# Kernel optimization log

Hardware: AMD Instinct MI355X
Metric: run time of the kernel (lower is better)

## Reference

```python
import math
import jax, jax.numpy as jnp
import numpy as np

WINDOW = 2  # LocalAttention default window_size
EPS = 1e-6


def _linear(x, W, b):
    return x @ W + b


def local_attention(x, Wq, bq, Wk, bk, Wv, bv):
    # x: [B, S, D]
    B, S, D = x.shape
    q = _linear(x, Wq, bq)
    k = _linear(x, Wk, bk)
    v = _linear(x, Wv, bv)
    idx = jnp.arange(S)
    # 0/1 banded mask -> softmax gives a dense row-stochastic matrix (faithful to source)
    mask = (jnp.abs(idx[:, None] - idx[None, :]) <= WINDOW).astype(x.dtype)  # [S, S]
    A = jax.nn.softmax(mask, axis=-1)  # [S, S]
    kk = jnp.einsum('st,btd->bsd', A, k)  # bmm(A, k)
    scores = jnp.einsum('bsd,btd->bst', q, kk) / math.sqrt(D)
    return jnp.einsum('bst,btd->bsd', jax.nn.softmax(scores, axis=-1), v)


def whole_norm(x, w, b):
    # LayerNorm with normalized_shape == full [B, S, D]: normalize over ALL elements
    mu = jnp.mean(x)
    var = jnp.mean(jnp.square(x - mu))
    return (x - mu) * jax.lax.rsqrt(var + EPS) * w + b


def ffn(x, W1, b1, W2, b2):
    return _linear(jax.nn.relu(_linear(x, W1, b1)), W2, b2)


def branch(feat, Wq, bq, Wk, bk, Wv, bv, W1, b1, W2, b2, nw, nb):
    out = local_attention(feat, Wq, bq, Wk, bk, Wv, bv)
    out = whole_norm(out + feat, nw, nb)
    out = ffn(out, W1, b1, W2, b2)
    return whole_norm(out + feat, nw, nb)


def _make_params(key, B, S, D):
    ks = jax.random.split(key, 5)
    s = 1.0 / math.sqrt(D)
    Wq = jax.random.normal(ks[0], (D, D), jnp.float32) * s
    Wk = jax.random.normal(ks[1], (D, D), jnp.float32) * s
    Wv = jax.random.normal(ks[2], (D, D), jnp.float32) * s
    W1 = jax.random.normal(ks[3], (D, 4 * D), jnp.float32) * s
    W2 = jax.random.normal(ks[4], (4 * D, D), jnp.float32) * (1.0 / math.sqrt(4 * D))
    return dict(Wq=Wq, bq=jnp.zeros((D,)), Wk=Wk, bk=jnp.zeros((D,)),
                Wv=Wv, bv=jnp.zeros((D,)), W1=W1, b1=jnp.zeros((4 * D,)),
                W2=W2, b2=jnp.zeros((D,)), nw=jnp.ones((B, S, D)), nb=jnp.zeros((B, S, D)))


def setup_inputs() -> dict:
    key = jax.random.key(0)
    k0, k1, k2, k3 = jax.random.split(key, 4)
    B, St, Dt = 8, 512, 1024
    Si, Di = 196, 768
    inp = {
        'text_feature': jax.random.normal(k0, (B, St, Dt), jnp.float32),
        'image_feature': jax.random.normal(k1, (B, Si, Di), jnp.float32),
    }
    tp = _make_params(k2, B, St, Dt)
    ip = _make_params(k3, B, Si, Di)
    for k, v in tp.items():
        inp['t_' + k] = v
    for k, v in ip.items():
        inp['i_' + k] = v
    return inp


def reference(text_feature, image_feature,
              t_Wq, t_bq, t_Wk, t_bk, t_Wv, t_bv, t_W1, t_b1, t_W2, t_b2, t_nw, t_nb,
              i_Wq, i_bq, i_Wk, i_bk, i_Wv, i_bv, i_W1, i_b1, i_W2, i_b2, i_nw, i_nb):
    image_out = branch(image_feature, i_Wq, i_bq, i_Wk, i_bk, i_Wv, i_bv,
                       i_W1, i_b1, i_W2, i_b2, i_nw, i_nb)
    text_out = branch(text_feature, t_Wq, t_bq, t_Wk, t_bk, t_Wv, t_bv,
                      t_W1, t_b1, t_W2, t_b2, t_nw, t_nb)
    return (text_out, image_out)
```

## Files before the change

### kernel.cpp

```cpp
#include <hip/hip_runtime.h>
#include <math.h>

typedef float  f32x4  __attribute__((ext_vector_type(4)));
typedef short  bf16x8 __attribute__((ext_vector_type(8)));

__device__ __forceinline__ unsigned short f2bf(float f) {
    union { float f; unsigned u; } v; v.f = f;
    unsigned u = v.u;
    return (unsigned short)((u + 0x7FFFu + ((u >> 16) & 1u)) >> 16);
}
__device__ __forceinline__ float bf2f(unsigned short u) {
    union { unsigned u; float f; } v; v.u = (unsigned)u << 16; return v.f;
}

#define GLOAD_LDS16(g, l)                                                      \
    __builtin_amdgcn_global_load_lds(                                          \
        (const __attribute__((address_space(1))) void*)(g),                    \
        (__attribute__((address_space(3))) void*)(l), 16, 0, 0)

template<int WRW, int WCW, int MR, int NR, bool OUT_BF16, bool RELU>
__global__ __launch_bounds__(512, 2)
void gemm5_bf16(const unsigned short* __restrict__ A,
                const unsigned short* __restrict__ BT,
                const float* __restrict__ bias, void* __restrict__ Cv,
                int M, int N, int K, int lda, int ldb, int ldc,
                long long sA, long long sB, long long sC, float alpha,
                int gx, int gy)
{
    constexpr int BK = 64;
    constexpr int WM = MR * 16, WN = NR * 16;
    constexpr int BM = WRW * WM, BN = WCW * WN;
    constexpr int NL = (BM + BN) / 64;
    __shared__ unsigned short Asm[2][BM * BK];
    __shared__ unsigned short Bsm[2][BN * BK];

    A  += (long long)blockIdx.z * sA;
    BT += (long long)blockIdx.z * sB;
    char* Cb = (char*)Cv + (long long)blockIdx.z * sC * (OUT_BF16 ? 2 : 4);

    const int nwg = gx * gy;
    int orig = blockIdx.x;
    int xcd = orig & 7, sidx = orig >> 3;
    int qq = nwg >> 3, rr = nwg & 7;
    int wg = (xcd < rr ? xcd * (qq + 1) : rr * (qq + 1) + (xcd - rr) * qq) + sidx;
    const int row0 = (wg / gx) * BM;
    const int col0 = (wg % gx) * BN;

    const int tid  = threadIdx.x;
    const int lane = tid & 63;
    const int wave = tid >> 6;
    const int wr   = wave / WCW;
    const int wc   = wave % WCW;

    const int lrow = lane & 15;
    const int cgrp = lane >> 4;

    f32x4 acc[MR][NR] = {};

    const int srl = tid >> 3;
    const int scl = (tid & 7) ^ (srl & 7);

    auto stage = [&](int buf, int k0) {
        #pragma unroll
        for (int is = 0; is < BM / 64; ++is)
            GLOAD_LDS16(A + (long long)(row0 + is * 64 + srl) * lda + (k0 + scl * 8),
                        &Asm[buf][is * 64 * BK + tid * 8]);
        #pragma unroll
        for (int is = 0; is < BN / 64; ++is)
            GLOAD_LDS16(BT + (long long)(col0 + is * 64 + srl) * ldb + (k0 + scl * 8),
                        &Bsm[buf][is * 64 * BK + tid * 8]);
    };

    const int nt = K / BK;
    stage(0, 0);

    for (int t = 0; t < nt; ++t) {
        const int cur = t & 1;
        if (t + 1 < nt) {
            stage(cur ^ 1, (t + 1) * BK);
            if constexpr (NL == 8)      asm volatile("s_waitcnt vmcnt(8)" ::: "memory");
            else if constexpr (NL == 6) asm volatile("s_waitcnt vmcnt(6)" ::: "memory");
            else                        asm volatile("s_waitcnt vmcnt(0)" ::: "memory");
        } else {
            asm volatile("s_waitcnt vmcnt(0)" ::: "memory");
        }
        __builtin_amdgcn_s_barrier();
        __builtin_amdgcn_sched_barrier(0);

        #pragma unroll
        for (int kk = 0; kk < 2; ++kk) {
            bf16x8 a_[MR], b_[NR];
            #pragma unroll
            for (int mf = 0; mf < MR; ++mf) {
                int row = wr * WM + mf * 16 + lrow;
                int phys = (kk * 4 + cgrp) ^ (row & 7);
                a_[mf] = *(const bf16x8*)&Asm[cur][row * BK + phys * 8];
            }
            #pragma unroll
            for (int nf = 0; nf < NR; ++nf) {
                int row = wc * WN + nf * 16 + lrow;
                int phys = (kk * 4 + cgrp) ^ (row & 7);
                b_[nf] = *(const bf16x8*)&Bsm[cur][row * BK + phys * 8];
            }
            __builtin_amdgcn_s_setprio(1);
            #pragma unroll
            for (int mf = 0; mf < MR; ++mf)
                #pragma unroll
                for (int nf = 0; nf < NR; ++nf)
                    acc[mf][nf] = __builtin_amdgcn_mfma_f32_16x16x32_bf16(
                        a_[mf], b_[nf], acc[mf][nf], 0, 0, 0);
            __builtin_amdgcn_s_setprio(0);
        }
        __builtin_amdgcn_s_barrier();
    }

    const int crow = cgrp * 4;
    const int ccol = lane & 15;
    #pragma unroll
    for (int mf = 0; mf < MR; ++mf) {
        int rbase = row0 + wr * WM + mf * 16 + crow;
        #pragma unroll
        for (int nf = 0; nf < NR; ++nf) {
            int c = col0 + wc * WN + nf * 16 + ccol;
            if (c >= N) continue;
            float bv = bias ? bias[c] : 0.f;
            #pragma unroll
            for (int j = 0; j < 4; ++j) {
                int r = rbase + j;
                if (r >= M) continue;
                float v = acc[mf][nf][j] * alpha + bv;
                if (RELU) v = fmaxf(v, 0.f);
                if (OUT_BF16)
                    ((unsigned short*)Cb)[(long long)r * ldc + c] = f2bf(v);
                else
                    ((float*)Cb)[(long long)r * ldc + c] = v;
            }
        }
    }
}

template<int WRW, int WCW, int MR, int NR>
static void gemm5_t(bool outBf16, bool relu,
                    const unsigned short* A, const unsigned short* BT, const float* bias,
                    void* C, int M, int N, int K, int lda, int ldb, int ldc,
                    int batch, long long sA, long long sB, long long sC,
                    float alpha, hipStream_t st)
{
    const int BM = WRW * MR * 16, BN = WCW * NR * 16;
    int gx = (N + BN - 1) / BN, gy = (M + BM - 1) / BM;
    dim3 grid(gx * gy, 1, batch);
    if (outBf16) {
        if (relu) gemm5_bf16<WRW, WCW, MR, NR, true , true ><<<grid, 512, 0, st>>>(A, BT, bias, C, M, N, K, lda, ldb, ldc, sA, sB, sC, alpha, gx, gy);
        else      gemm5_bf16<WRW, WCW, MR, NR, true , false><<<grid, 512, 0, st>>>(A, BT, bias, C, M, N, K, lda, ldb, ldc, sA, sB, sC, alpha, gx, gy);
    } else {
        if (relu) gemm5_bf16<WRW, WCW, MR, NR, false, true ><<<grid, 512, 0, st>>>(A, BT, bias, C, M, N, K, lda, ldb, ldc, sA, sB, sC, alpha, gx, gy);
        else      gemm5_bf16<WRW, WCW, MR, NR, false, false><<<grid, 512, 0, st>>>(A, BT, bias, C, M, N, K, lda, ldb, ldc, sA, sB, sC, alpha, gx, gy);
    }
}

template<int MR, int NR, bool OUT_BF16, bool RELU>
__global__ __launch_bounds__(512, 4)
void gemm4_bf16(const unsigned short* __restrict__ A,
                const unsigned short* __restrict__ BT,
                const float* __restrict__ bias, void* __restrict__ Cv,
                int M, int N, int K, int lda, int ldb, int ldc,
                long long sA, long long sB, long long sC, float alpha,
                int gx, int gy)
{
    constexpr int BK = 64;
    constexpr int WM = MR * 16, WN = NR * 16;
    constexpr int BM = 2 * WM, BN = 4 * WN;
    __shared__ unsigned short Asm[2][BM * BK];
    __shared__ unsigned short Bsm[2][BN * BK];

    A  += (long long)blockIdx.z * sA;
    BT += (long long)blockIdx.z * sB;
    char* Cb = (char*)Cv + (long long)blockIdx.z * sC * (OUT_BF16 ? 2 : 4);

    const int nwg = gx * gy;
    int orig = blockIdx.x;
    int xcd = orig & 7, sidx = orig >> 3;
    int qq = nwg >> 3, rr = nwg & 7;
    int wg = (xcd < rr ? xcd * (qq + 1) : rr * (qq + 1) + (xcd - rr) * qq) + sidx;
    const int row0 = (wg / gx) * BM;
    const int col0 = (wg % gx) * BN;

    const int tid  = threadIdx.x;
    const int lane = tid & 63;
    const int wave = tid >> 6;
    const int wr   = wave >> 2;
    const int wc   = wave & 3;

    const int lrow = lane & 15;
    const int cgrp = lane >> 4;

    f32x4 acc[MR][NR] = {};

    const int srl = tid >> 3;
    const int scl = (tid & 7) ^ (srl & 7);

    auto stage = [&](int buf, int k0) {
        #pragma unroll
        for (int is = 0; is < BM / 64; ++is)
            GLOAD_LDS16(A + (long long)(row0 + is * 64 + srl) * lda + (k0 + scl * 8),
                        &Asm[buf][is * 64 * BK + tid * 8]);
        #pragma unroll
        for (int is = 0; is < BN / 64; ++is)
            GLOAD_LDS16(BT + (long long)(col0 + is * 64 + srl) * ldb + (k0 + scl * 8),
                        &Bsm[buf][is * 64 * BK + tid * 8]);
    };

    const int nt = K / BK;
    stage(0, 0);
    __syncthreads();

    for (int t = 0; t < nt; ++t) {
        if (t + 1 < nt) stage((t + 1) & 1, (t + 1) * BK);
        const int cur = t & 1;

        bf16x8 a_[2][MR], b_[2][NR];
        #pragma unroll
        for (int kk = 0; kk < 2; ++kk) {
            #pragma unroll
            for (int mf = 0; mf < MR; ++mf) {
                int row = wr * WM + mf * 16 + lrow;
                int phys = (kk * 4 + cgrp) ^ (row & 7);
                a_[kk][mf] = *(const bf16x8*)&Asm[cur][row * BK + phys * 8];
            }
            #pragma unroll
            for (int nf = 0; nf < NR; ++nf) {
                int row = wc * WN + nf * 16 + lrow;
                int phys = (kk * 4 + cgrp) ^ (row & 7);
                b_[kk][nf] = *(const bf16x8*)&Bsm[cur][row * BK + phys * 8];
            }
        }

        __builtin_amdgcn_s_setprio(1);
        #pragma unroll
        for (int kk = 0; kk < 2; ++kk)
            #pragma unroll
            for (int mf = 0; mf < MR; ++mf)
                #pragma unroll
                for (int nf = 0; nf < NR; ++nf)
                    acc[mf][nf] = __builtin_amdgcn_mfma_f32_16x16x32_bf16(
                        a_[kk][mf], b_[kk][nf], acc[mf][nf], 0, 0, 0);
        __builtin_amdgcn_s_setprio(0);

        __syncthreads();
    }

    const int crow = cgrp * 4;
    const int ccol = lane & 15;
    #pragma unroll
    for (int mf = 0; mf < MR; ++mf) {
        int rbase = row0 + wr * WM + mf * 16 + crow;
        #pragma unroll
        for (int nf = 0; nf < NR; ++nf) {
            int c = col0 + wc * WN + nf * 16 + ccol;
            if (c >= N) continue;
            float bv = bias ? bias[c] : 0.f;
            #pragma unroll
            for (int j = 0; j < 4; ++j) {
                int r = rbase + j;
                if (r >= M) continue;
                float v = acc[mf][nf][j] * alpha + bv;
                if (RELU) v = fmaxf(v, 0.f);
                if (OUT_BF16)
                    ((unsigned short*)Cb)[(long long)r * ldc + c] = f2bf(v);
                else
                    ((float*)Cb)[(long long)r * ldc + c] = v;
            }
        }
    }
}

template<int MR, int NR>
static void gemm4_t(bool outBf16, bool relu,
                    const unsigned short* A, const unsigned short* BT, const float* bias,
                    void* C, int M, int N, int K, int lda, int ldb, int ldc,
                    int batch, long long sA, long long sB, long long sC,
                    float alpha, hipStream_t st)
{
    const int BM = 2 * MR * 16, BN = 4 * NR * 16;
    int gx = (N + BN - 1) / BN, gy = (M + BM - 1) / BM;
    dim3 grid(gx * gy, 1, batch);
    if (outBf16) {
        if (relu) gemm4_bf16<MR, NR, true , true ><<<grid, 512, 0, st>>>(A, BT, bias, C, M, N, K, lda, ldb, ldc, sA, sB, sC, alpha, gx, gy);
        else      gemm4_bf16<MR, NR, true , false><<<grid, 512, 0, st>>>(A, BT, bias, C, M, N, K, lda, ldb, ldc, sA, sB, sC, alpha, gx, gy);
    } else {
        if (relu) gemm4_bf16<MR, NR, false, true ><<<grid, 512, 0, st>>>(A, BT, bias, C, M, N, K, lda, ldb, ldc, sA, sB, sC, alpha, gx, gy);
        else      gemm4_bf16<MR, NR, false, false><<<grid, 512, 0, st>>>(A, BT, bias, C, M, N, K, lda, ldb, ldc, sA, sB, sC, alpha, gx, gy);
    }
}

template<int BM, int BN, bool OUT_BF16>
__global__ __launch_bounds__(256)
void gemm_bf16(const unsigned short* __restrict__ A,
               const unsigned short* __restrict__ BT,
               const float* __restrict__ bias, void* __restrict__ Cv,
               int M, int N, int K, int lda, int ldb, int ldc,
               long long sA, long long sB, long long sC, float alpha,
               int gx, int gy)
{
    constexpr int BK = 32;
    constexpr int WM = BM / 2, WN = BN / 2;
    constexpr int MR = WM / 16, NR = WN / 16;
    __shared__ unsigned short Asm[BM * BK];
    __shared__ unsigned short Bsm[BN * BK];

    A  += (long long)blockIdx.z * sA;
    BT += (long long)blockIdx.z * sB;
    char* Cb = (char*)Cv + (long long)blockIdx.z * sC * (OUT_BF16 ? 2 : 4);

    const int nwg = gx * gy;
    int orig = blockIdx.x;
    int xcd = orig & 7, sidx = orig >> 3;
    int qq = nwg >> 3, rr = nwg & 7;
    int wg = (xcd < rr ? xcd * (qq + 1) : rr * (qq + 1) + (xcd - rr) * qq) + sidx;
    const int row0 = (wg % gy) * BM;
    const int col0 = (wg / gy) * BN;

    const int tid  = threadIdx.x;
    const int lane = tid & 63;
    const int wave = tid >> 6;
    const int wr   = wave >> 1;
    const int wc   = wave & 1;

    const int srow = tid >> 2;
    const int skel = (tid & 3) * 8;

    f32x4 acc[MR][NR] = {};

    const int lrow = lane & 15;
    const int lk   = (lane >> 4) * 8;

    for (int k0 = 0; k0 < K; k0 += BK) {
        #pragma unroll
        for (int is = 0; is < BM / 64; ++is)
            GLOAD_LDS16(A + (long long)(row0 + is * 64 + srow) * lda + (k0 + skel),
                        &Asm[(is * 64 + srow) * BK + skel]);
        #pragma unroll
        for (int is = 0; is < BN / 64; ++is)
            GLOAD_LDS16(BT + (long long)(col0 + is * 64 + srow) * ldb + (k0 + skel),
                        &Bsm[(is * 64 + srow) * BK + skel]);
        __syncthreads();

        bf16x8 af[MR], bfr[NR];
        #pragma unroll
        for (int mf = 0; mf < MR; ++mf)
            af[mf] = *(const bf16x8*)&Asm[(wr * WM + mf * 16 + lrow) * BK + lk];
        #pragma unroll
        for (int nf = 0; nf < NR; ++nf)
            bfr[nf] = *(const bf16x8*)&Bsm[(wc * WN + nf * 16 + lrow) * BK + lk];
        #pragma unroll
        for (int mf = 0; mf < MR; ++mf)
            #pragma unroll
            for (int nf = 0; nf < NR; ++nf)
                acc[mf][nf] = __builtin_amdgcn_mfma_f32_16x16x32_bf16(
                    af[mf], bfr[nf], acc[mf][nf], 0, 0, 0);
        __syncthreads();
    }

    const int crow = (lane >> 4) * 4;
    const int ccol = lane & 15;
    #pragma unroll
    for (int mf = 0; mf < MR; ++mf) {
        int rbase = row0 + wr * WM + mf * 16 + crow;
        #pragma unroll
        for (int nf = 0; nf < NR; ++nf) {
            int c = col0 + wc * WN + nf * 16 + ccol;
            if (c >= N) continue;
            float bv = bias ? bias[c] : 0.f;
            #pragma unroll
            for (int j = 0; j < 4; ++j) {
                int r = rbase + j;
                if (r >= M) continue;
                float v = acc[mf][nf][j] * alpha + bv;
                if (OUT_BF16)
                    ((unsigned short*)Cb)[(long long)r * ldc + c] = f2bf(v);
                else
                    ((float*)Cb)[(long long)r * ldc + c] = v;
            }
        }
    }
}

template<int BM, int BN>
static void gemm_t(bool outBf16,
                   const unsigned short* A, const unsigned short* BT, const float* bias,
                   void* C, int M, int N, int K, int lda, int ldb, int ldc,
                   int batch, long long sA, long long sB, long long sC,
                   float alpha, hipStream_t st)
{
    int gx = (N + BN - 1) / BN, gy = (M + BM - 1) / BM;
    dim3 grid(gx * gy, 1, batch);
    if (outBf16)
        gemm_bf16<BM, BN, true ><<<grid, 256, 0, st>>>(A, BT, bias, C, M, N, K, lda, ldb, ldc, sA, sB, sC, alpha, gx, gy);
    else
        gemm_bf16<BM, BN, false><<<grid, 256, 0, st>>>(A, BT, bias, C, M, N, K, lda, ldb, ldc, sA, sB, sC, alpha, gx, gy);
}

__global__ void splitk_stats_kernel(const float4* __restrict__ part,
                                    const float4* __restrict__ bias,
                                    const float4* __restrict__ x,
                                    float4* __restrict__ z,
                                    double* __restrict__ dpart,
                                    long long n4, int N4, int nsplit, long long stride4)
{
    __shared__ double rs[256], rs2[256];
    int tid = threadIdx.x;
    long long i = (long long)blockIdx.x * blockDim.x + tid;
    long long gs = (long long)gridDim.x * blockDim.x;
    double s = 0.0, s2 = 0.0;
    for (; i < n4; i += gs) {
        float4 a = part[i];
        for (int sp = 1; sp < nsplit; ++sp) {
            float4 b = part[(long long)sp * stride4 + i];
            a.x += b.x; a.y += b.y; a.z += b.z; a.w += b.w;
        }
        float4 bv = bias[(int)(i % N4)];
        float4 xv = x[i];
        a.x += bv.x + xv.x; a.y += bv.y + xv.y; a.z += bv.z + xv.z; a.w += bv.w + xv.w;
        z[i] = a;
        s  += (double)a.x + (double)a.y + (double)a.z + (double)a.w;
        s2 += (double)a.x * a.x + (double)a.y * a.y + (double)a.z * a.z + (double)a.w * a.w;
    }
    rs[tid] = s; rs2[tid] = s2; __syncthreads();
    for (int k = 128; k > 0; k >>= 1) {
        if (tid < k) { rs[tid] += rs[tid + k]; rs2[tid] += rs2[tid + k]; }
        __syncthreads();
    }
    if (tid == 0) { dpart[2 * blockIdx.x] = rs[0]; dpart[2 * blockIdx.x + 1] = rs2[0]; }
}

__global__ void norm_apply_z_kernel(const float4* __restrict__ z,
                                    const float4* __restrict__ nw, const float4* __restrict__ nb,
                                    const float* __restrict__ stats, float4* __restrict__ out,
                                    long long n4)
{
    float mu = stats[0], rstd = stats[1];
    long long i = (long long)blockIdx.x * blockDim.x + threadIdx.x;
    long long stride = (long long)gridDim.x * blockDim.x;
    for (; i < n4; i += stride) {
        float4 zv = z[i], wv = nw[i], bv = nb[i];
        float4 o;
        o.x = (zv.x - mu) * rstd * wv.x + bv.x;
        o.y = (zv.y - mu) * rstd * wv.y + bv.y;
        o.z = (zv.z - mu) * rstd * wv.z + bv.z;
        o.w = (zv.w - mu) * rstd * wv.w + bv.w;
        out[i] = o;
    }
}

__global__ void cast_bf16_kernel(const float4* __restrict__ in,
                                 ushort4* __restrict__ out, long long n4)
{
    long long i = (long long)blockIdx.x * blockDim.x + threadIdx.x;
    long long stride = (long long)gridDim.x * blockDim.x;
    for (; i < n4; i += stride) {
        float4 v = in[i];
        ushort4 o;
        o.x = f2bf(v.x); o.y = f2bf(v.y); o.z = f2bf(v.z); o.w = f2bf(v.w);
        out[i] = o;
    }
}

__global__ void transpose_cast_kernel(const float* __restrict__ src,
                                      unsigned short* __restrict__ dst,
                                      int R, int C, int Rpad,
                                      long long sSrc, long long sDst)
{
    __shared__ float t[32][33];
    src += (long long)blockIdx.z * sSrc;
    dst += (long long)blockIdx.z * sDst;
    int r0 = blockIdx.x * 32, c0 = blockIdx.y * 32;
    int tx = threadIdx.x & 31, ty = threadIdx.x >> 5;
    #pragma unroll
    for (int i = 0; i < 32; i += 8) {
        int r = r0 + ty + i, c = c0 + tx;
        t[ty + i][tx] = (r < R && c < C) ? src[(long long)r * C + c] : 0.f;
    }
    __syncthreads();
    #pragma unroll
    for (int i = 0; i < 32; i += 8) {
        int c = c0 + ty + i, r = r0 + tx;
        if (c < C && r < Rpad)
            dst[(long long)c * Rpad + r] = f2bf(t[tx][ty + i]);
    }
}

__global__ void transpose_bf16_kernel(const unsigned short* __restrict__ src,
                                      unsigned short* __restrict__ dst,
                                      int R, int C, int Rpad, int ldS,
                                      long long sSrc, long long sDst)
{
    __shared__ unsigned short t[32][33];
    src += (long long)blockIdx.z * sSrc;
    dst += (long long)blockIdx.z * sDst;
    int r0 = blockIdx.x * 32, c0 = blockIdx.y * 32;
    int tx = threadIdx.x & 31, ty = threadIdx.x >> 5;
    #pragma unroll
    for (int i = 0; i < 32; i += 8) {
        int r = r0 + ty + i, c = c0 + tx;
        t[ty + i][tx] = (r < R && c < C) ? src[(long long)r * ldS + c] : (unsigned short)0;
    }
    __syncthreads();
    #pragma unroll
    for (int i = 0; i < 32; i += 8) {
        int c = c0 + ty + i, r = r0 + tx;
        if (c < C && r < Rpad)
            dst[(long long)c * Rpad + r] = t[tx][ty + i];
    }
}

#define KTOT_NCH 16
__global__ void ktot_partial_bf16(const unsigned short* __restrict__ k,
                                  float* __restrict__ part,
                                  int B, int S, int D, int ld)
{
    int bch = blockIdx.x;
    int b  = bch / KTOT_NCH;
    int ch = bch % KTOT_NCH;
    int d  = blockIdx.y * 256 + threadIdx.x;
    if (d >= D) return;
    int len = (S + KTOT_NCH - 1) / KTOT_NCH;
    int lo = ch * len;
    int hi = lo + len < S ? lo + len : S;
    const unsigned short* kp = k + ((long long)b * S + lo) * ld + d;
    float s = 0.f;
    for (int t = lo; t < hi; ++t, kp += ld) s += bf2f(*kp);
    part[(long long)bch * D + d] = s;
}

__global__ void ktot_finish_kernel(const float* __restrict__ part,
                                   float* __restrict__ ktot, int B, int D)
{
    int idx = blockIdx.x * blockDim.x + threadIdx.x;
    if (idx >= B * D) return;
    int b = idx / D, d = idx % D;
    float s = 0.f;
    #pragma unroll
    for (int ch = 0; ch < KTOT_NCH; ++ch)
        s += part[((long long)b * KTOT_NCH + ch) * D + d];
    ktot[idx] = s;
}

__global__ void kk_bf16_kernel(const unsigned short* __restrict__ k,
                               const float* __restrict__ ktot,
                               unsigned short* __restrict__ kk,
                               int B, int S, int D, int ld)
{
    long long idx = (long long)blockIdx.x * blockDim.x + threadIdx.x;
    int D4 = D >> 2;
    long long n4 = (long long)B * S * D4;
    if (idx >= n4) return;
    int d4 = (int)(idx % D4);
    long long bs = idx / D4;
    int s = (int)(bs % S);
    int b = (int)(bs / S);
    int lo = s - 2 > 0 ? s - 2 : 0;
    int hi = s + 2 < S - 1 ? s + 2 : S - 1;
    int c = hi - lo + 1;
    const float E = 2.718281828459045f;
    float Zinv = 1.f / ((float)(S - c) + E * (float)c);

    float w0 = 0.f, w1 = 0.f, w2 = 0.f, w3 = 0.f;
    const unsigned short* kp = k + ((long long)b * S + lo) * ld + d4 * 4;
    for (int t = lo; t <= hi; ++t, kp += ld) {
        ushort4 kv = *(const ushort4*)kp;
        w0 += bf2f(kv.x); w1 += bf2f(kv.y); w2 += bf2f(kv.z); w3 += bf2f(kv.w);
    }
    float4 tot = *((const float4*)(ktot + b * D) + d4);
    ushort4 o;
    o.x = f2bf((tot.x + (E - 1.f) * w0) * Zinv);
    o.y = f2bf((tot.y + (E - 1.f) * w1) * Zinv);
    o.z = f2bf((tot.z + (E - 1.f) * w2) * Zinv);
    o.w = f2bf((tot.w + (E - 1.f) * w3) * Zinv);
    ((ushort4*)(kk + ((long long)b * S + s) * D))[d4] = o;
}

__global__ void softmax_rows_bf16(const float* __restrict__ sc,
                                  unsigned short* __restrict__ P, int S, int Spad)
{
    long long row = blockIdx.x;
    const float* p = sc + row * (long long)Spad;
    unsigned short* o = P + row * (long long)Spad;
    int tid = threadIdx.x;
    __shared__ float red[256];

    float m = -INFINITY;
    for (int t = tid; t < S; t += 256) m = fmaxf(m, p[t]);
    red[tid] = m; __syncthreads();
    for (int s = 128; s > 0; s >>= 1) {
        if (tid < s) red[tid] = fmaxf(red[tid], red[tid + s]);
        __syncthreads();
    }
    m = red[0];
    __syncthreads();

    float sum = 0.f;
    for (int t = tid; t < S; t += 256) sum += __expf(p[t] - m);
    red[tid] = sum; __syncthreads();
    for (int s = 128; s > 0; s >>= 1) {
        if (tid < s) red[tid] += red[tid + s];
        __syncthreads();
    }
    float inv = 1.f / red[0];
    for (int t = tid; t < Spad; t += 256)
        o[t] = (t < S) ? f2bf(__expf(p[t] - m) * inv) : (unsigned short)0;
}

__global__ void stats_kernel(const float4* __restrict__ a, const float4* __restrict__ f,
                             double* __restrict__ part, long long n4)
{
    __shared__ double rs[256], rs2[256];
    int tid = threadIdx.x;
    long long i = (long long)blockIdx.x * blockDim.x + tid;
    long long stride = (long long)gridDim.x * blockDim.x;
    double s = 0.0, s2 = 0.0;
    for (; i < n4; i += stride) {
        float4 av = a[i], fv = f[i];
        float z0 = av.x + fv.x, z1 = av.y + fv.y, z2 = av.z + fv.z, z3 = av.w + fv.w;
        s  += (double)z0 + (double)z1 + (double)z2 + (double)z3;
        s2 += (double)z0 * z0 + (double)z1 * z1 + (double)z2 * z2 + (double)z3 * z3;
    }
    rs[tid] = s; rs2[tid] = s2; __syncthreads();
    for (int k = 128; k > 0; k >>= 1) {
        if (tid < k) { rs[tid] += rs[tid + k]; rs2[tid] += rs2[tid + k]; }
        __syncthreads();
    }
    if (tid == 0) { part[2 * blockIdx.x] = rs[0]; part[2 * blockIdx.x + 1] = rs2[0]; }
}

__global__ void finish_stats(const double* __restrict__ part, int npart,
                             float* __restrict__ stats, double n)
{
    __shared__ double rs[256], rs2[256];
    int tid = threadIdx.x;
    double s = 0.0, s2 = 0.0;
    for (int i = tid; i < npart; i += 256) { s += part[2 * i]; s2 += part[2 * i + 1]; }
    rs[tid] = s; rs2[tid] = s2; __syncthreads();
    for (int k = 128; k > 0; k >>= 1) {
        if (tid < k) { rs[tid] += rs[tid + k]; rs2[tid] += rs2[tid + k]; }
        __syncthreads();
    }
    if (tid == 0) {
        double mu  = rs[0] / n;
        double var = rs2[0] / n - mu * mu;
        stats[0] = (float)mu;
        stats[1] = (float)(1.0 / sqrt(var + 1e-6));
    }
}

__global__ void norm_apply_kernel(const float4* __restrict__ a, const float4* __restrict__ f,
                                  const float4* __restrict__ nw, const float4* __restrict__ nb,
                                  const float* __restrict__ stats, ushort4* __restrict__ out,
                                  long long n4)
{
    float mu = stats[0], rstd = stats[1];
    long long i = (long long)blockIdx.x * blockDim.x + threadIdx.x;
    long long stride = (long long)gridDim.x * blockDim.x;
    for (; i < n4; i += stride) {
        float4 av = a[i], fv = f[i], wv = nw[i], bv = nb[i];
        ushort4 o;
        o.x = f2bf((av.x + fv.x - mu) * rstd * wv.x + bv.x);
        o.y = f2bf((av.y + fv.y - mu) * rstd * wv.y + bv.y);
        o.z = f2bf((av.z + fv.z - mu) * rstd * wv.z + bv.z);
        o.w = f2bf((av.w + fv.w - mu) * rstd * wv.w + bv.w);
        out[i] = o;
    }
}

struct Bufs {
    unsigned short *xb, *qkv, *kkb, *vT, *P, *h, *WqkvT, *W1T, *W2T;
    float *f32buf, *bqkv, *ktot, *ktot_part, *stats;
    double *part;
};

static void run_branch(const float* x, const float* const* w, bool big,
                       float* out, int B, int S, int D, const Bufs& wsb, hipStream_t st)
{
    const float *Wq = w[0], *bq = w[1], *Wk = w[2], *bk = w[3], *Wv = w[4], *bv = w[5];
    const float *W1 = w[6], *b1 = w[7], *W2 = w[8], *b2 = w[9], *nw = w[10], *nb = w[11];

    const int Spad = (S + 31) & ~31;
    const long long M = (long long)B * S;
    const long long n = M * D;
    const long long n4 = n / 4;
    const float inv_sqrt_d = (float)(1.0 / sqrt((double)D));
    const int D3 = 3 * D, D4 = 4 * D;

    unsigned short* y1b = wsb.kkb;
    float* scores = (float*)wsb.h;
    float* splitbuf = (float*)wsb.qkv;

    cast_bf16_kernel<<<1024, 256, 0, st>>>((const float4*)x, (ushort4*)wsb.xb, n4);
    transpose_cast_kernel<<<dim3((D + 31) / 32, (D + 31) / 32, 1), 256, 0, st>>>(Wq, wsb.WqkvT,               D, D, D, 0, 0);
    transpose_cast_kernel<<<dim3((D + 31) / 32, (D + 31) / 32, 1), 256, 0, st>>>(Wk, wsb.WqkvT + (long long)D * D, D, D, D, 0, 0);
    transpose_cast_kernel<<<dim3((D + 31) / 32, (D + 31) / 32, 1), 256, 0, st>>>(Wv, wsb.WqkvT + 2LL * D * D, D, D, D, 0, 0);
    transpose_cast_kernel<<<dim3((D + 31) / 32, (D4 + 31) / 32, 1), 256, 0, st>>>(W1, wsb.W1T, D, D4, D, 0, 0);
    transpose_cast_kernel<<<dim3((D4 + 31) / 32, (D + 31) / 32, 1), 256, 0, st>>>(W2, wsb.W2T, D4, D, D4, 0, 0);
    hipMemcpyAsync(wsb.bqkv,         bq, D * sizeof(float), hipMemcpyDeviceToDevice, st);
    hipMemcpyAsync(wsb.bqkv + D,     bk, D * sizeof(float), hipMemcpyDeviceToDevice, st);
    hipMemcpyAsync(wsb.bqkv + 2 * D, bv, D * sizeof(float), hipMemcpyDeviceToDevice, st);

    if (big)
        gemm5_t<2, 4, 8, 4>(true, false, wsb.xb, wsb.WqkvT, wsb.bqkv, wsb.qkv,
                            (int)M, D3, D, D, D, D3, 1, 0, 0, 0, 1.f, st);
    else
        gemm4_t<4, 2>(true, false, wsb.xb, wsb.WqkvT, wsb.bqkv, wsb.qkv,
                      (int)M, D3, D, D, D, D3, 1, 0, 0, 0, 1.f, st);

    const unsigned short* kcol = wsb.qkv + D;
    ktot_partial_bf16<<<dim3(B * KTOT_NCH, (D + 255) / 256), 256, 0, st>>>(kcol, wsb.ktot_part, B, S, D, D3);
    ktot_finish_kernel<<<(B * D + 255) / 256, 256, 0, st>>>(wsb.ktot_part, wsb.ktot, B, D);
    kk_bf16_kernel<<<(int)((n4 + 255) / 256), 256, 0, st>>>(kcol, wsb.ktot, wsb.kkb, B, S, D, D3);

    transpose_bf16_kernel<<<dim3((Spad + 31) / 32, (D + 31) / 32, B), 256, 0, st>>>(
        wsb.qkv + 2 * D, wsb.vT, S, D, Spad, D3, (long long)S * D3, (long long)D * Spad);

    gemm_t<64, 64>(false, wsb.qkv, wsb.kkb, nullptr, scores, S, S, D, D3, D, Spad,
                   B, (long long)S * D3, (long long)S * D, (long long)S * Spad, inv_sqrt_d, st);
    softmax_rows_bf16<<<(int)M, 256, 0, st>>>(scores, wsb.P, S, Spad);

    gemm_t<128, 64>(false, wsb.P, wsb.vT, nullptr, wsb.f32buf, S, D, Spad, Spad, Spad, D,
                    B, (long long)S * Spad, (long long)D * Spad, (long long)S * D, 1.f, st);

    stats_kernel<<<1024, 256, 0, st>>>((const float4*)wsb.f32buf, (const float4*)x, wsb.part, n4);
    finish_stats<<<1, 256, 0, st>>>(wsb.part, 1024, wsb.stats, (double)n);
    norm_apply_kernel<<<2048, 256, 0, st>>>((const float4*)wsb.f32buf, (const float4*)x,
        (const float4*)nw, (const float4*)nb, wsb.stats, (ushort4*)y1b, n4);

    if (big)
        gemm5_t<2, 4, 8, 4>(true, true, y1b, wsb.W1T, b1, wsb.h,
                            (int)M, D4, D, D, D, D4, 1, 0, 0, 0, 1.f, st);
    else
        gemm4_t<4, 2>(true, true, y1b, wsb.W1T, b1, wsb.h, (int)M, D4, D, D, D, D4, 1, 0, 0, 0, 1.f, st);

    {
        int nsplit = big ? 2 : 8;
        int Ksp = D4 / nsplit;
        if (big)
            gemm5_t<4, 2, 4, 4>(false, false, wsb.h, wsb.W2T, nullptr, splitbuf,
                                (int)M, D, Ksp, D4, D4, D,
                                nsplit, Ksp, Ksp, M * D, 1.f, st);
        else
            gemm4_t<4, 2>(false, false, wsb.h, wsb.W2T, nullptr, splitbuf,
                          (int)M, D, Ksp, D4, D4, D,
                          nsplit, Ksp, Ksp, M * D, 1.f, st);
        splitk_stats_kernel<<<1024, 256, 0, st>>>((const float4*)splitbuf, (const float4*)b2,
                                                  (const float4*)x, (float4*)wsb.f32buf,
                                                  wsb.part, n4, D / 4, nsplit, n4);
        finish_stats<<<1, 256, 0, st>>>(wsb.part, 1024, wsb.stats, (double)n);
        norm_apply_z_kernel<<<2048, 256, 0, st>>>((const float4*)wsb.f32buf,
            (const float4*)nw, (const float4*)nb, wsb.stats, (float4*)out, n4);
    }
}

extern "C" void kernel_launch(void* const* d_in, const int* in_sizes, int n_in,
                              void* d_out, int out_size, void* d_ws, size_t ws_size,
                              hipStream_t stream)
{
    const float* text  = (const float*)d_in[0];
    const float* image = (const float*)d_in[1];
    const float* tw[12];
    const float* iw[12];
    for (int i = 0; i < 12; ++i) tw[i] = (const float*)d_in[2 + i];
    for (int i = 0; i < 12; ++i) iw[i] = (const float*)d_in[14 + i];

    float* out_text = (float*)d_out;
    float* out_img  = out_text + 8LL * 512 * 1024;

    char* p = (char*)d_ws;
    auto alloc = [&](long long bytes) {
        char* r = p;
        p += (bytes + 255) & ~255LL;
        return r;
    };
    const long long MD  = 4096LL * 1024;
    const long long BDS = 8LL * 1024 * 512;
    const long long SS  = 8LL * 512 * 512;
    Bufs b;
    b.xb      = (unsigned short*)alloc(MD * 2);
    b.qkv     = (unsigned short*)alloc(MD * 3 * 2);
    b.kkb     = (unsigned short*)alloc(MD * 2);
    b.vT      = (unsigned short*)alloc(BDS * 2);
    b.P       = (unsigned short*)alloc(SS * 2);
    b.h       = (unsigned short*)alloc(MD * 4 * 2);
    b.WqkvT   = (unsigned short*)alloc(3LL * 1024 * 1024 * 2);
    b.W1T     = (unsigned short*)alloc(4096LL * 1024 * 2);
    b.W2T     = (unsigned short*)alloc(4096LL * 1024 * 2);
    b.f32buf  = (float*)alloc(MD * 4);
    b.bqkv    = (float*)alloc(3LL * 1024 * 4);
    b.ktot    = (float*)alloc(8192LL * 4);
    b.ktot_part = (float*)alloc(8192LL * KTOT_NCH * 4);
    b.part    = (double*)alloc(2048LL * 8);
    b.stats   = (float*)alloc(256);

    run_branch(text,  tw, true,  out_text, 8, 512, 1024, b, stream);
    run_branch(image, iw, false, out_img,  8, 196, 768,  b, stream);
}
```

Baseline: 491.5 us.

## Replace big-branch GEMM with 256-thread BK=32 kernel and drop gemm5 for W2

The 512-thread, BK=64 gemm5 kernel with hand-tuned vmcnt waits is replaced by a 4-wave gemm6 kernel. It uses a 256x128 tile, BK=32, a 4-way XOR swizzle and plain __syncthreads double buffering. The QKV and W1 GEMMs for the text branch use the new kernel, and the split-K W2 GEMM for the text branch falls back to gemm4. The aim is simpler scheduling and better occupancy, at the cost of twice as many K iterations and barriers and weaker load/compute overlap, since the explicit partial waitcnt is gone.

```diff
diff --git a/kernel.cpp b/kernel.cpp
--- a/kernel.cpp
+++ b/kernel.cpp
@@ -18,19 +18,19 @@
         (const __attribute__((address_space(1))) void*)(g),                    \
         (__attribute__((address_space(3))) void*)(l), 16, 0, 0)
 
-template<int WRW, int WCW, int MR, int NR, bool OUT_BF16, bool RELU>
-__global__ __launch_bounds__(512, 2)
-void gemm5_bf16(const unsigned short* __restrict__ A,
+template<bool OUT_BF16, bool RELU>
+__global__ __launch_bounds__(256, 2)
+void gemm6_bf16(const unsigned short* __restrict__ A,
                 const unsigned short* __restrict__ BT,
                 const float* __restrict__ bias, void* __restrict__ Cv,
                 int M, int N, int K, int lda, int ldb, int ldc,
                 long long sA, long long sB, long long sC, float alpha,
                 int gx, int gy)
 {
-    constexpr int BK = 64;
+    constexpr int BK = 32;
+    constexpr int MR = 8, NR = 4;
     constexpr int WM = MR * 16, WN = NR * 16;
-    constexpr int BM = WRW * WM, BN = WCW * WN;
-    constexpr int NL = (BM + BN) / 64;
+    constexpr int BM = 2 * WM, BN = 2 * WN;
     __shared__ unsigned short Asm[2][BM * BK];
     __shared__ unsigned short Bsm[2][BN * BK];
 
@@ -49,16 +49,16 @@
     const int tid  = threadIdx.x;
     const int lane = tid & 63;
     const int wave = tid >> 6;
-    const int wr   = wave / WCW;
-    const int wc   = wave % WCW;
+    const int wr   = wave >> 1;
+    const int wc   = wave & 1;
 
     const int lrow = lane & 15;
     const int cgrp = lane >> 4;
 
     f32x4 acc[MR][NR] = {};
 
-    const int srl = tid >> 3;
-    const int scl = (tid & 7) ^ (srl & 7);
+    const int srl  = tid >> 2;
+    const int scl  = (tid & 3) ^ (srl & 3);
 
     auto stage = [&](int buf, int k0) {
         #pragma unroll
@@ -73,45 +73,36 @@
 
     const int nt = K / BK;
     stage(0, 0);
+    __syncthreads();
 
     for (int t = 0; t < nt; ++t) {
+        if (t + 1 < nt) stage((t + 1) & 1, (t + 1) * BK);
         const int cur = t & 1;
-        if (t + 1 < nt) {
-            stage(cur ^ 1, (t + 1) * BK);
-            if constexpr (NL == 8)      asm volatile("s_waitcnt vmcnt(8)" ::: "memory");
-            else if constexpr (NL == 6) asm volatile("s_waitcnt vmcnt(6)" ::: "memory");
-            else                        asm volatile("s_waitcnt vmcnt(0)" ::: "memory");
-        } else {
-            asm volatile("s_waitcnt vmcnt(0)" ::: "memory");
+
+        bf16x8 a_[MR], b_[NR];
+        #pragma unroll
+        for (int mf = 0; mf < MR; ++mf) {
+            int row = wr * WM + mf * 16 + lrow;
+            int phys = cgrp ^ (row & 3);
+            a_[mf] = *(const bf16x8*)&Asm[cur][row * BK + phys * 8];
         }
-        __builtin_amdgcn_s_barrier();
-        __builtin_amdgcn_sched_barrier(0);
-
-        #pragma unroll
-        for (int kk = 0; kk < 2; ++kk) {
-            bf16x8 a_[MR], b_[NR];
+        #pragma unroll
+        for (int nf = 0; nf < NR; ++nf) {
+            int row = wc * WN + nf * 16 + lrow;
+            int phys = cgrp ^ (row & 3);
+            b_[nf] = *(const bf16x8*)&Bsm[cur][row * BK + phys * 8];
+        }
+
+        __builtin_amdgcn_s_setprio(1);
+        #pragma unroll
+        for (int mf = 0; mf < MR; ++mf)
             #pragma unroll
-            for (int mf = 0; mf < MR; ++mf) {
-                int row = wr * WM + mf * 16 + lrow;
-                int phys = (kk * 4 + cgrp) ^ (row & 7);
-                a_[mf] = *(const bf16x8*)&Asm[cur][row * BK + phys * 8];
-            }
-            #pragma unroll
-            for (int nf = 0; nf < NR; ++nf) {
-                int row = wc * WN + nf * 16 + lrow;
-                int phys = (kk * 4 + cgrp) ^ (row & 7);
-                b_[nf] = *(const bf16x8*)&Bsm[cur][row * BK + phys * 8];
-            }
-            __builtin_amdgcn_s_setprio(1);
-            #pragma unroll
-            for (int mf = 0; mf < MR; ++mf)
-                #pragma unroll
-                for (int nf = 0; nf < NR; ++nf)
-                    acc[mf][nf] = __builtin_amdgcn_mfma_f32_16x16x32_bf16(
-                        a_[mf], b_[nf], acc[mf][nf], 0, 0, 0);
-            __builtin_amdgcn_s_setprio(0);
-        }
-        __builtin_amdgcn_s_barrier();
+            for (int nf = 0; nf < NR; ++nf)
+                acc[mf][nf] = __builtin_amdgcn_mfma_f32_16x16x32_bf16(
+                    a_[mf], b_[nf], acc[mf][nf], 0, 0, 0);
+        __builtin_amdgcn_s_setprio(0);
+
+        __syncthreads();
     }
 
     const int crow = cgrp * 4;
@@ -139,22 +130,21 @@
     }
 }
 
-template<int WRW, int WCW, int MR, int NR>
-static void gemm5_t(bool outBf16, bool relu,
+static void gemm6_t(bool outBf16, bool relu,
                     const unsigned short* A, const unsigned short* BT, const float* bias,
                     void* C, int M, int N, int K, int lda, int ldb, int ldc,
                     int batch, long long sA, long long sB, long long sC,
                     float alpha, hipStream_t st)
 {
-    const int BM = WRW * MR * 16, BN = WCW * NR * 16;
+    const int BM = 256, BN = 128;
     int gx = (N + BN - 1) / BN, gy = (M + BM - 1) / BM;
     dim3 grid(gx * gy, 1, batch);
     if (outBf16) {
-        if (relu) gemm5_bf16<WRW, WCW, MR, NR, true , true ><<<grid, 512, 0, st>>>(A, BT, bias, C, M, N, K, lda, ldb, ldc, sA, sB, sC, alpha, gx, gy);
-        else      gemm5_bf16<WRW, WCW, MR, NR, true , false><<<grid, 512, 0, st>>>(A, BT, bias, C, M, N, K, lda, ldb, ldc, sA, sB, sC, alpha, gx, gy);
+        if (relu) gemm6_bf16<true , true ><<<grid, 256, 0, st>>>(A, BT, bias, C, M, N, K, lda, ldb, ldc, sA, sB, sC, alpha, gx, gy);
+        else      gemm6_bf16<true , false><<<grid, 256, 0, st>>>(A, BT, bias, C, M, N, K, lda, ldb, ldc, sA, sB, sC, alpha, gx, gy);
     } else {
-        if (relu) gemm5_bf16<WRW, WCW, MR, NR, false, true ><<<grid, 512, 0, st>>>(A, BT, bias, C, M, N, K, lda, ldb, ldc, sA, sB, sC, alpha, gx, gy);
-        else      gemm5_bf16<WRW, WCW, MR, NR, false, false><<<grid, 512, 0, st>>>(A, BT, bias, C, M, N, K, lda, ldb, ldc, sA, sB, sC, alpha, gx, gy);
+        if (relu) gemm6_bf16<false, true ><<<grid, 256, 0, st>>>(A, BT, bias, C, M, N, K, lda, ldb, ldc, sA, sB, sC, alpha, gx, gy);
+        else      gemm6_bf16<false, false><<<grid, 256, 0, st>>>(A, BT, bias, C, M, N, K, lda, ldb, ldc, sA, sB, sC, alpha, gx, gy);
     }
 }
 
@@ -705,8 +695,8 @@
     hipMemcpyAsync(wsb.bqkv + 2 * D, bv, D * sizeof(float), hipMemcpyDeviceToDevice, st);
 
     if (big)
-        gemm5_t<2, 4, 8, 4>(true, false, wsb.xb, wsb.WqkvT, wsb.bqkv, wsb.qkv,
-                            (int)M, D3, D, D, D, D3, 1, 0, 0, 0, 1.f, st);
+        gemm6_t(true, false, wsb.xb, wsb.WqkvT, wsb.bqkv, wsb.qkv,
+                (int)M, D3, D, D, D, D3, 1, 0, 0, 0, 1.f, st);
     else
         gemm4_t<4, 2>(true, false, wsb.xb, wsb.WqkvT, wsb.bqkv, wsb.qkv,
                       (int)M, D3, D, D, D, D3, 1, 0, 0, 0, 1.f, st);
@@ -732,22 +722,17 @@
         (const float4*)nw, (const float4*)nb, wsb.stats, (ushort4*)y1b, n4);
 
     if (big)
-        gemm5_t<2, 4, 8, 4>(true, true, y1b, wsb.W1T, b1, wsb.h,
-                            (int)M, D4, D, D, D, D4, 1, 0, 0, 0, 1.f, st);
+        gemm6_t(true, true, y1b, wsb.W1T, b1, wsb.h,
+                (int)M, D4, D, D, D, D4, 1, 0, 0, 0, 1.f, st);
     else
         gemm4_t<4, 2>(true, true, y1b, wsb.W1T, b1, wsb.h, (int)M, D4, D, D, D, D4, 1, 0, 0, 0, 1.f, st);
 
     {
         int nsplit = big ? 2 : 8;
         int Ksp = D4 / nsplit;
-        if (big)
-            gemm5_t<4, 2, 4, 4>(false, false, wsb.h, wsb.W2T, nullptr, splitbuf,
-                                (int)M, D, Ksp, D4, D4, D,
-                                nsplit, Ksp, Ksp, M * D, 1.f, st);
-        else
-            gemm4_t<4, 2>(false, false, wsb.h, wsb.W2T, nullptr, splitbuf,
-                          (int)M, D, Ksp, D4, D4, D,
-                          nsplit, Ksp, Ksp, M * D, 1.f, st);
+        gemm4_t<4, 2>(false, false, wsb.h, wsb.W2T, nullptr, splitbuf,
+                      (int)M, D, Ksp, D4, D4, D,
+                      nsplit, Ksp, Ksp, M * D, 1.f, st);
         splitk_stats_kernel<<<1024, 256, 0, st>>>((const float4*)splitbuf, (const float4*)b2,
                                                   (const float4*)x, (float4*)wsb.f32buf,
                                                   wsb.part, n4, D / 4, nsplit, n4);
```

New measurement: 480.4 us. 2.3% less time.
